# Kernel optimization log

Hardware: AMD Instinct MI355X
Metric: run time of the kernel (lower is better)

The kernel has to match this reference:

```python
import jax, jax.numpy as jnp
import numpy as np

D_HEAD = 64
SCALE = 1.0 / (D_HEAD ** 0.5)
MASK_VALUE = -1e9


def setup_inputs() -> dict:
    key = jax.random.key(0)
    kq, kk, kv, km = jax.random.split(key, 4)
    B, H, S, D = 2, 12, 2048, D_HEAD
    Q = jax.random.normal(kq, (B, H, S, D), dtype=jnp.float32)
    K = jax.random.normal(kk, (B, H, S, D), dtype=jnp.float32)
    V = jax.random.normal(kv, (B, H, S, D), dtype=jnp.float32)
    attn_mask = jax.random.randint(km, (B, 1, S, S), 0, 2).astype(bool)
    return {"Q": Q, "K": K, "V": V, "attn_mask": attn_mask}


def reference(Q, K, V, attn_mask):
    # scores: [B,H,S,S]
    scores = jnp.einsum('bhqd,bhkd->bhqk', Q, K) * SCALE
    scores = jnp.where(attn_mask, MASK_VALUE, scores)
    attn_prob = jax.nn.softmax(scores, axis=-1)
    # dropout p=0.0 (eval mode) -> identity
    context = jnp.einsum('bhqk,bhkd->bhqd', attn_prob, V)
    return (context, attn_prob)
```

## Files before the change

kernel.cpp:

```cpp
#include <hip/hip_runtime.h>
#include <hip/hip_bf16.h>
#include <math.h>

#define B_SZ   2
#define NH     12
#define S_LEN  2048
#define D_HD   64
#define NQ_EL  ((size_t)B_SZ * NH * S_LEN * D_HD)

typedef __attribute__((ext_vector_type(8))) __bf16 bf16x8;
typedef __attribute__((ext_vector_type(4))) __bf16 bf16x4;
typedef __attribute__((ext_vector_type(4))) float  f32x4;
typedef __attribute__((ext_vector_type(4))) unsigned u32x4;

__device__ __forceinline__ int detect_mask_mode64(const void* mask) {
  const int lane = threadIdx.x & 63;
  unsigned v = ((const unsigned*)mask)[lane];
  if (__ballot(v <= 1u) == ~0ull) return 0;
  if (__ballot(v == 0u || v == 0x3f800000u) == ~0ull) return 2;
  unsigned h0 = v & 0xFFFFu, h1 = v >> 16;
  bool okb = (h0 == 0u || h0 == 0x3f80u) && (h1 == 0u || h1 == 0x3f80u);
  if (__ballot(okb) == ~0ull) return 3;
  return 1;
}

__device__ __forceinline__ bool mask_at(const void* mask, int mode, size_t idx) {
  if (mode == 0) return ((const int*)mask)[idx] != 0;
  if (mode == 1) return ((const unsigned char*)mask)[idx] != 0;
  if (mode == 2) return ((const float*)mask)[idx] != 0.0f;
  return ((const unsigned short*)mask)[idx] != 0;
}

__global__ __launch_bounds__(256)
void prep_kernel(const float* __restrict__ Q, const float* __restrict__ K,
                 const float* __restrict__ V, const void* __restrict__ mask,
                 unsigned* __restrict__ bits, __bf16* __restrict__ Qb,
                 __bf16* __restrict__ Kb, __bf16* __restrict__ VT) {
  const int blk = blockIdx.x;
  const int tid = threadIdx.x;
  if (blk < 512) {
    const int mode = detect_mask_mode64(mask);
    const int lane = tid & 63;
#pragma unroll 4
    for (int i = 0; i < 64; ++i) {
      const size_t idx = ((size_t)blk * 64 + i) * 256 + tid;
      const unsigned long long bal = __ballot(mask_at(mask, mode, idx));
      if (lane == 0)       bits[idx >> 5] = (unsigned)bal;
      else if (lane == 32) bits[idx >> 5] = (unsigned)(bal >> 32);
    }
  } else if (blk < 1536) {
    const bool isq = blk < 1024;
    const float* src = isq ? Q : K;
    __bf16* dst = isq ? Qb : Kb;
    const float scale = isq ? 0.125f : 1.0f;
    const size_t base = (size_t)(blk & 511) * 256 + tid;
#pragma unroll
    for (int i = 0; i < 6; ++i) {
      const size_t li = base + (size_t)i * 512 * 256;
      float4 a = ((const float4*)src)[li];
      __bf16 o0 = (__bf16)(a.x * scale), o1 = (__bf16)(a.y * scale);
      __bf16 o2 = (__bf16)(a.z * scale), o3 = (__bf16)(a.w * scale);
      ((ushort4*)dst)[li] = (ushort4){
          __builtin_bit_cast(unsigned short, o0), __builtin_bit_cast(unsigned short, o1),
          __builtin_bit_cast(unsigned short, o2), __builtin_bit_cast(unsigned short, o3)};
    }
  } else {
    __shared__ __align__(16) __bf16 tl[D_HD][72];
    const int t  = blk - 1536;
    const int bh = t >> 5;
    const int k0 = (t & 31) * 64;
#pragma unroll
    for (int i = 0; i < 4; ++i) {
      const int vi = i * 256 + tid;
      const int kk = vi >> 4, dv = (vi & 15) * 4;
      float4 f = *(const float4*)(V + ((size_t)bh * S_LEN + k0 + kk) * D_HD + dv);
      tl[dv + 0][kk] = (__bf16)f.x; tl[dv + 1][kk] = (__bf16)f.y;
      tl[dv + 2][kk] = (__bf16)f.z; tl[dv + 3][kk] = (__bf16)f.w;
    }
    __syncthreads();
#pragma unroll
    for (int half = 0; half < 2; ++half) {
      const int d = half * 32 + (tid >> 3);
      const int kc = (tid & 7) * 8;
      bf16x8 vv = *(const bf16x8*)&tl[d][kc];
      *(bf16x8*)(VT + ((size_t)bh * D_HD + d) * S_LEN + k0 + kc) = vv;
    }
  }
}

__device__ __forceinline__ bf16x8 ld8f(const float* p, float scale) {
  const float4 a = *(const float4*)p;
  const float4 b = *(const float4*)(p + 4);
  bf16x8 r;
  r[0] = (__bf16)(a.x * scale); r[1] = (__bf16)(a.y * scale);
  r[2] = (__bf16)(a.z * scale); r[3] = (__bf16)(a.w * scale);
  r[4] = (__bf16)(b.x * scale); r[5] = (__bf16)(b.y * scale);
  r[6] = (__bf16)(b.z * scale); r[7] = (__bf16)(b.w * scale);
  return r;
}

__global__ __launch_bounds__(512, 4)
void attn_main(const __bf16* __restrict__ Qb, const __bf16* __restrict__ Kb,
               const __bf16* __restrict__ VT, const unsigned* __restrict__ mbits,
               float* __restrict__ out_ctx)
{
  float* out_p = out_ctx + NQ_EL;

  const int flat = blockIdx.x + blockIdx.y * gridDim.x;
  const int wf   = (flat & 7) * 384 + (flat >> 3);
  const int bh   = wf >> 7;
  const int qg   = wf & 127;
  const int b    = bh / NH;

  const int tid  = threadIdx.x;
  const int lane = tid & 63;
  const int w    = tid >> 6;
  const int qbase = qg * 16;
  const int col  = lane & 15;
  const int g    = lane >> 4;
  const int q    = qbase + col;
  const int k0   = w * 256;

  const size_t mbase = ((size_t)b * S_LEN + q) * (S_LEN / 32);

  const size_t qoff = ((size_t)bh * S_LEN + q) * D_HD + g * 8;
  const bf16x8 bq0 = *(const bf16x8*)(Qb + qoff);
  const bf16x8 bq1 = *(const bf16x8*)(Qb + qoff + 32);

  __shared__ float lsh[8][16];
  __shared__ float linv_s[16];
  __shared__ float csum[8][16][66];

  unsigned pe[8][4];
  float lsum = 0.f;
#pragma unroll
  for (int c = 0; c < 8; ++c) {
    const int kc = k0 + c * 32;
    const unsigned mw = mbits[mbase + (kc >> 5)];
    float e[8];
#pragma unroll
    for (int sub = 0; sub < 2; ++sub) {
      const int kb = kc + sub * 16;
      const size_t koff = ((size_t)bh * S_LEN + kb + col) * D_HD + g * 8;
      bf16x8 ak0 = *(const bf16x8*)(Kb + koff);
      bf16x8 ak1 = *(const bf16x8*)(Kb + koff + 32);
      f32x4 acc = {0.f, 0.f, 0.f, 0.f};
      acc = __builtin_amdgcn_mfma_f32_16x16x32_bf16(ak0, bq0, acc, 0, 0, 0);
      acc = __builtin_amdgcn_mfma_f32_16x16x32_bf16(ak1, bq1, acc, 0, 0, 0);
#pragma unroll
      for (int r = 0; r < 4; ++r) {
        const bool msk = (mw >> (sub * 16 + g * 4 + r)) & 1;
        float ev = msk ? 0.f : __expf(acc[r]);
        e[sub * 4 + r] = ev;
        lsum += ev;
      }
    }
#pragma unroll
    for (int j = 0; j < 4; ++j) {
      unsigned lo = __builtin_bit_cast(unsigned short, (__bf16)e[2 * j]);
      unsigned hi = __builtin_bit_cast(unsigned short, (__bf16)e[2 * j + 1]);
      pe[c][j] = (hi << 16) | lo;
    }
  }
  lsum += __shfl_xor(lsum, 16);
  lsum += __shfl_xor(lsum, 32);
  if (lane < 16) lsh[w][col] = lsum;
  __syncthreads();
  float tot = 0.f;
#pragma unroll
  for (int w8 = 0; w8 < 8; ++w8) tot += lsh[w8][col];
  const float inv_l = 1.0f / tot;
  if (w == 0 && lane < 16) linv_s[col] = inv_l;

  f32x4 cacc[4];
#pragma unroll
  for (int dt = 0; dt < 4; dt++) cacc[dt] = (f32x4){0.f, 0.f, 0.f, 0.f};

  float* prow = out_p + (size_t)bh * S_LEN * S_LEN + (size_t)q * S_LEN + k0;
  const __bf16* vbase = VT + (size_t)bh * D_HD * S_LEN;

#pragma unroll
  for (int c = 0; c < 8; ++c) {
    const int kc = k0 + c * 32;
    bf16x8 vf[4];
#pragma unroll
    for (int dt = 0; dt < 4; dt++) {
      const __bf16* vrow = vbase + (size_t)(dt * 16 + col) * S_LEN + kc;
      bf16x4 lo = *(const bf16x4*)(vrow + g * 4);
      bf16x4 hi = *(const bf16x4*)(vrow + 16 + g * 4);
      vf[dt] = __builtin_shufflevector(lo, hi, 0, 1, 2, 3, 4, 5, 6, 7);
    }
#pragma unroll
    for (int sub = 0; sub < 2; ++sub) {
      f32x4 st;
      unsigned u0 = pe[c][sub * 2 + 0], u1 = pe[c][sub * 2 + 1];
      st[0] = __builtin_bit_cast(float, u0 << 16) * inv_l;
      st[1] = __builtin_bit_cast(float, u0 & 0xFFFF0000u) * inv_l;
      st[2] = __builtin_bit_cast(float, u1 << 16) * inv_l;
      st[3] = __builtin_bit_cast(float, u1 & 0xFFFF0000u) * inv_l;
      __builtin_nontemporal_store(st, (f32x4*)(prow + c * 32 + sub * 16 + g * 4));
    }
    u32x4 w4 = {pe[c][0], pe[c][1], pe[c][2], pe[c][3]};
    bf16x8 pa = __builtin_bit_cast(bf16x8, w4);
#pragma unroll
    for (int dt = 0; dt < 4; dt++)
      cacc[dt] = __builtin_amdgcn_mfma_f32_16x16x32_bf16(pa, vf[dt], cacc[dt], 0, 0, 0);
  }

#pragma unroll
  for (int dt = 0; dt < 4; dt++)
#pragma unroll
    for (int r = 0; r < 4; r++)
      csum[w][g * 4 + r][dt * 16 + col] = cacc[dt][r];
  __syncthreads();
  {
    const int qo = tid >> 5;
    const int d0 = (tid * 2) & 63;
    float s0 = 0.f, s1 = 0.f;
#pragma unroll
    for (int w8 = 0; w8 < 8; ++w8) {
      s0 += csum[w8][qo][d0];
      s1 += csum[w8][qo][d0 + 1];
    }
    const float lv = linv_s[qo];
    float2 o = {s0 * lv, s1 * lv};
    *(float2*)(out_ctx + ((size_t)bh * S_LEN + qbase + qo) * D_HD + d0) = o;
  }
}

template<bool USE_BITS>
__global__ __launch_bounds__(512)
void attn_fb(const float* __restrict__ Qg, const float* __restrict__ Kg,
             const float* __restrict__ Vg, const void* __restrict__ mask,
             const unsigned* __restrict__ mbits, float* __restrict__ out_ctx)
{
  float* out_p = out_ctx + NQ_EL;
  const int flat = blockIdx.x + blockIdx.y * gridDim.x;
  const int wf   = (flat & 7) * 96 + (flat >> 3);
  const int qt = wf & 31, bh = wf >> 5, b = bh / NH;
  const int tid = threadIdx.x, lane = tid & 63, w = tid >> 6;
  const int qw = w & 3, kh = w >> 2;
  const int qbase = qt * 64 + qw * 16;
  const int col = lane & 15, g = lane >> 4;
  const int q = qbase + col;
  const int k0 = kh * (S_LEN / 2);
  int mmode = 0;
  if constexpr (!USE_BITS) mmode = detect_mask_mode64(mask);
  const size_t mrow  = (size_t)b * S_LEN * S_LEN;
  const size_t mbase = ((size_t)b * S_LEN + q) * (S_LEN / 32);
  const size_t qoff = ((size_t)bh * S_LEN + q) * D_HD + g * 8;
  const bf16x8 bq0 = ld8f(Qg + qoff, 0.125f);
  const bf16x8 bq1 = ld8f(Qg + qoff + 32, 0.125f);

  float lsum = 0.f;
  for (int kc = k0; kc < k0 + S_LEN / 2; kc += 32) {
    unsigned mw = 0;
    if constexpr (USE_BITS) mw = mbits[mbase + (kc >> 5)];
#pragma unroll
    for (int sub = 0; sub < 2; ++sub) {
      const int kb = kc + sub * 16;
      const size_t koff = ((size_t)bh * S_LEN + kb + col) * D_HD + g * 8;
      bf16x8 ak0 = ld8f(Kg + koff, 1.0f);
      bf16x8 ak1 = ld8f(Kg + koff + 32, 1.0f);
      f32x4 acc = {0.f, 0.f, 0.f, 0.f};
      acc = __builtin_amdgcn_mfma_f32_16x16x32_bf16(ak0, bq0, acc, 0, 0, 0);
      acc = __builtin_amdgcn_mfma_f32_16x16x32_bf16(ak1, bq1, acc, 0, 0, 0);
#pragma unroll
      for (int r = 0; r < 4; ++r) {
        bool msk;
        if constexpr (USE_BITS) msk = (mw >> (sub * 16 + g * 4 + r)) & 1;
        else msk = mask_at(mask, mmode, mrow + (size_t)q * S_LEN + kb + g * 4 + r);
        lsum += msk ? 0.f : __expf(acc[r]);
      }
    }
  }
  lsum += __shfl_xor(lsum, 16);
  lsum += __shfl_xor(lsum, 32);
  __shared__ float lsh[8][16];
  __shared__ float csum[4][16][66];
  if (lane < 16) lsh[w][col] = lsum;
  __syncthreads();
  const float inv_l = 1.0f / (lsum + lsh[w ^ 4][col]);

  f32x4 cacc[4];
#pragma unroll
  for (int dt = 0; dt < 4; dt++) cacc[dt] = (f32x4){0.f, 0.f, 0.f, 0.f};
  float* prow = out_p + (size_t)bh * S_LEN * S_LEN + (size_t)q * S_LEN;

  for (int it = 0; it < S_LEN / 64; ++it) {
    const int kc = k0 + it * 32;
    unsigned mw = 0;
    if constexpr (USE_BITS) mw = mbits[mbase + (kc >> 5)];
    float p[8];
#pragma unroll
    for (int sub = 0; sub < 2; ++sub) {
      const int kb = kc + sub * 16;
      const size_t koff = ((size_t)bh * S_LEN + kb + col) * D_HD + g * 8;
      bf16x8 ak0 = ld8f(Kg + koff, 1.0f);
      bf16x8 ak1 = ld8f(Kg + koff + 32, 1.0f);
      f32x4 acc = {0.f, 0.f, 0.f, 0.f};
      acc = __builtin_amdgcn_mfma_f32_16x16x32_bf16(ak0, bq0, acc, 0, 0, 0);
      acc = __builtin_amdgcn_mfma_f32_16x16x32_bf16(ak1, bq1, acc, 0, 0, 0);
#pragma unroll
      for (int r = 0; r < 4; ++r) {
        bool msk;
        if constexpr (USE_BITS) msk = (mw >> (sub * 16 + g * 4 + r)) & 1;
        else msk = mask_at(mask, mmode, mrow + (size_t)q * S_LEN + kb + g * 4 + r);
        p[sub * 4 + r] = msk ? 0.f : __expf(acc[r]) * inv_l;
      }
      float4 st = {p[sub * 4 + 0], p[sub * 4 + 1], p[sub * 4 + 2], p[sub * 4 + 3]};
      *(float4*)(prow + kb + g * 4) = st;
    }
    bf16x8 pa;
#pragma unroll
    for (int e = 0; e < 8; e++) pa[e] = (__bf16)p[e];
#pragma unroll
    for (int dt = 0; dt < 4; dt++) {
      bf16x8 vf;
#pragma unroll
      for (int e = 0; e < 8; e++) {
        const int kidx = kc + (e >> 2) * 16 + g * 4 + (e & 3);
        vf[e] = (__bf16)Vg[((size_t)bh * S_LEN + kidx) * D_HD + dt * 16 + col];
      }
      cacc[dt] = __builtin_amdgcn_mfma_f32_16x16x32_bf16(pa, vf, cacc[dt], 0, 0, 0);
    }
  }
  if (kh == 1) {
#pragma unroll
    for (int dt = 0; dt < 4; dt++)
#pragma unroll
      for (int r = 0; r < 4; r++)
        csum[qw][g * 4 + r][dt * 16 + col] = cacc[dt][r];
  }
  __syncthreads();
  if (kh == 0) {
#pragma unroll
    for (int dt = 0; dt < 4; dt++)
#pragma unroll
      for (int r = 0; r < 4; r++)
        out_ctx[((size_t)bh * S_LEN + qbase + g * 4 + r) * D_HD + dt * 16 + col] =
            cacc[dt][r] + csum[qw][g * 4 + r][dt * 16 + col];
  }
}

__global__ __launch_bounds__(256)
void build_bits_kernel(const void* __restrict__ mask, unsigned* __restrict__ bits) {
  const int mode = detect_mask_mode64(mask);
  const size_t i = (size_t)blockIdx.x * 256 + threadIdx.x;
  const unsigned long long bal = __ballot(mask_at(mask, mode, i));
  const int lane = threadIdx.x & 63;
  if (lane == 0)       bits[i >> 5] = (unsigned)bal;
  else if (lane == 32) bits[i >> 5] = (unsigned)(bal >> 32);
}

extern "C" void kernel_launch(void* const* d_in, const int* in_sizes, int n_in,
                              void* d_out, int out_size, void* d_ws, size_t ws_size,
                              hipStream_t stream) {
  const float* Q = (const float*)d_in[0];
  const float* K = (const float*)d_in[1];
  const float* V = (const float*)d_in[2];
  const void* mask = d_in[3];
  float* out = (float*)d_out;

  const size_t mask_elems = (size_t)B_SZ * S_LEN * S_LEN;
  const size_t off_bits = 256;
  const size_t off_q  = off_bits + mask_elems / 8;
  const size_t off_k  = off_q + NQ_EL * 2;
  const size_t off_vt = off_k + NQ_EL * 2;
  const size_t need   = off_vt + NQ_EL * 2;

  if (ws_size >= need) {
    unsigned* bits = (unsigned*)((char*)d_ws + off_bits);
    __bf16* Qb = (__bf16*)((char*)d_ws + off_q);
    __bf16* Kb = (__bf16*)((char*)d_ws + off_k);
    __bf16* VT = (__bf16*)((char*)d_ws + off_vt);
    prep_kernel<<<2304, 256, 0, stream>>>(Q, K, V, mask, bits, Qb, Kb, VT);
    dim3 grid(128, 24);
    attn_main<<<grid, 512, 0, stream>>>(Qb, Kb, VT, bits, out);
  } else if (ws_size >= off_q) {
    unsigned* bits = (unsigned*)((char*)d_ws + off_bits);
    build_bits_kernel<<<(unsigned)(mask_elems / 256), 256, 0, stream>>>(mask, bits);
    dim3 gfb(S_LEN / 64, B_SZ * NH);
    attn_fb<true><<<gfb, 512, 0, stream>>>(Q, K, V, mask, bits, out);
  } else {
    dim3 gfb(S_LEN / 64, B_SZ * NH);
    attn_fb<false><<<gfb, 512, 0, stream>>>(Q, K, V, mask, nullptr, out);
  }
}
```

Baseline: 327.5 us.

## Prefetch K tiles one chunk ahead and coalesce attn_prob stores via lane shuffles

K fragments and mask words for the next 32-key chunk are now loaded one iteration early, so global-load latency overlaps the current chunk's MFMAs and exps. The probability write-out is reorganized: lanes exchange packed bf16 values with shuffles so that eight consecutive lanes write 128 contiguous bytes of one query row, replacing strided 16-byte stores that were scattered across 16 rows. The stores also change from nontemporal to regular. This costs extra shuffles, extra registers for the prefetched tiles, and recomputed per-row inverse sums.

```diff
diff --git a/kernel.cpp b/kernel.cpp
--- a/kernel.cpp
+++ b/kernel.cpp
@@ -99,6 +99,13 @@
   return r;
 }
 
+__device__ __forceinline__ float bflo(unsigned u) {
+  return __builtin_bit_cast(float, u << 16);
+}
+__device__ __forceinline__ float bfhi(unsigned u) {
+  return __builtin_bit_cast(float, u & 0xFFFF0000u);
+}
+
 __global__ __launch_bounds__(512, 4)
 void attn_main(const __bf16* __restrict__ Qb, const __bf16* __restrict__ Kb,
                const __bf16* __restrict__ VT, const unsigned* __restrict__ mbits,
@@ -122,8 +129,9 @@
   const int k0   = w * 256;
 
   const size_t mbase = ((size_t)b * S_LEN + q) * (S_LEN / 32);
-
-  const size_t qoff = ((size_t)bh * S_LEN + q) * D_HD + g * 8;
+  const size_t khead = (size_t)bh * S_LEN;
+
+  const size_t qoff = (khead + q) * D_HD + g * 8;
   const bf16x8 bq0 = *(const bf16x8*)(Qb + qoff);
   const bf16x8 bq1 = *(const bf16x8*)(Qb + qoff + 32);
 
@@ -133,26 +141,53 @@
 
   unsigned pe[8][4];
   float lsum = 0.f;
+
+  bf16x8 nk0a, nk0b, nk1a, nk1b;
+  {
+    const size_t koff0 = (khead + k0 + col) * D_HD + g * 8;
+    const size_t koff1 = (khead + k0 + 16 + col) * D_HD + g * 8;
+    nk0a = *(const bf16x8*)(Kb + koff0);
+    nk0b = *(const bf16x8*)(Kb + koff0 + 32);
+    nk1a = *(const bf16x8*)(Kb + koff1);
+    nk1b = *(const bf16x8*)(Kb + koff1 + 32);
+  }
+  unsigned nmw = mbits[mbase + (k0 >> 5)];
+
 #pragma unroll
   for (int c = 0; c < 8; ++c) {
-    const int kc = k0 + c * 32;
-    const unsigned mw = mbits[mbase + (kc >> 5)];
+    const bf16x8 k0a = nk0a, k0b = nk0b, k1a = nk1a, k1b = nk1b;
+    const unsigned mw = nmw;
+    if (c < 7) {
+      const int kn = k0 + (c + 1) * 32;
+      const size_t koff0 = (khead + kn + col) * D_HD + g * 8;
+      const size_t koff1 = (khead + kn + 16 + col) * D_HD + g * 8;
+      nk0a = *(const bf16x8*)(Kb + koff0);
+      nk0b = *(const bf16x8*)(Kb + koff0 + 32);
+      nk1a = *(const bf16x8*)(Kb + koff1);
+      nk1b = *(const bf16x8*)(Kb + koff1 + 32);
+      nmw = mbits[mbase + (kn >> 5)];
+    }
     float e[8];
-#pragma unroll
-    for (int sub = 0; sub < 2; ++sub) {
-      const int kb = kc + sub * 16;
-      const size_t koff = ((size_t)bh * S_LEN + kb + col) * D_HD + g * 8;
-      bf16x8 ak0 = *(const bf16x8*)(Kb + koff);
-      bf16x8 ak1 = *(const bf16x8*)(Kb + koff + 32);
+    {
       f32x4 acc = {0.f, 0.f, 0.f, 0.f};
-      acc = __builtin_amdgcn_mfma_f32_16x16x32_bf16(ak0, bq0, acc, 0, 0, 0);
-      acc = __builtin_amdgcn_mfma_f32_16x16x32_bf16(ak1, bq1, acc, 0, 0, 0);
+      acc = __builtin_amdgcn_mfma_f32_16x16x32_bf16(k0a, bq0, acc, 0, 0, 0);
+      acc = __builtin_amdgcn_mfma_f32_16x16x32_bf16(k0b, bq1, acc, 0, 0, 0);
 #pragma unroll
       for (int r = 0; r < 4; ++r) {
-        const bool msk = (mw >> (sub * 16 + g * 4 + r)) & 1;
-        float ev = msk ? 0.f : __expf(acc[r]);
-        e[sub * 4 + r] = ev;
-        lsum += ev;
+        const bool msk = (mw >> (g * 4 + r)) & 1;
+        e[r] = msk ? 0.f : __expf(acc[r]);
+        lsum += e[r];
+      }
+    }
+    {
+      f32x4 acc = {0.f, 0.f, 0.f, 0.f};
+      acc = __builtin_amdgcn_mfma_f32_16x16x32_bf16(k1a, bq0, acc, 0, 0, 0);
+      acc = __builtin_amdgcn_mfma_f32_16x16x32_bf16(k1b, bq1, acc, 0, 0, 0);
+#pragma unroll
+      for (int r = 0; r < 4; ++r) {
+        const bool msk = (mw >> (16 + g * 4 + r)) & 1;
+        e[4 + r] = msk ? 0.f : __expf(acc[r]);
+        lsum += e[4 + r];
       }
     }
 #pragma unroll
@@ -166,17 +201,29 @@
   lsum += __shfl_xor(lsum, 32);
   if (lane < 16) lsh[w][col] = lsum;
   __syncthreads();
-  float tot = 0.f;
-#pragma unroll
-  for (int w8 = 0; w8 < 8; ++w8) tot += lsh[w8][col];
-  const float inv_l = 1.0f / tot;
-  if (w == 0 && lane < 16) linv_s[col] = inv_l;
+  {
+    float tot = 0.f;
+#pragma unroll
+    for (int w8 = 0; w8 < 8; ++w8) tot += lsh[w8][col];
+    if (w == 0 && lane < 16) linv_s[col] = 1.0f / tot;
+  }
+  const int Lr = lane >> 3;
+  const int u  = lane & 7;
+  float linv_t[2];
+#pragma unroll
+  for (int t = 0; t < 2; ++t) {
+    float tot = 0.f;
+#pragma unroll
+    for (int w8 = 0; w8 < 8; ++w8) tot += lsh[w8][t * 8 + Lr];
+    linv_t[t] = 1.0f / tot;
+  }
+  const int subg = u >> 2;
 
   f32x4 cacc[4];
 #pragma unroll
   for (int dt = 0; dt < 4; dt++) cacc[dt] = (f32x4){0.f, 0.f, 0.f, 0.f};
 
-  float* prow = out_p + (size_t)bh * S_LEN * S_LEN + (size_t)q * S_LEN + k0;
+  float* pblk = out_p + (size_t)bh * S_LEN * S_LEN + (size_t)qbase * S_LEN + k0;
   const __bf16* vbase = VT + (size_t)bh * D_HD * S_LEN;
 
 #pragma unroll
@@ -191,14 +238,17 @@
       vf[dt] = __builtin_shufflevector(lo, hi, 0, 1, 2, 3, 4, 5, 6, 7);
     }
 #pragma unroll
-    for (int sub = 0; sub < 2; ++sub) {
-      f32x4 st;
-      unsigned u0 = pe[c][sub * 2 + 0], u1 = pe[c][sub * 2 + 1];
-      st[0] = __builtin_bit_cast(float, u0 << 16) * inv_l;
-      st[1] = __builtin_bit_cast(float, u0 & 0xFFFF0000u) * inv_l;
-      st[2] = __builtin_bit_cast(float, u1 << 16) * inv_l;
-      st[3] = __builtin_bit_cast(float, u1 & 0xFFFF0000u) * inv_l;
-      __builtin_nontemporal_store(st, (f32x4*)(prow + c * 32 + sub * 16 + g * 4));
+    for (int t = 0; t < 2; ++t) {
+      const int src = 16 * (u & 3) + t * 8 + Lr;
+      unsigned a0 = (unsigned)__shfl((int)pe[c][0], src);
+      unsigned a1 = (unsigned)__shfl((int)pe[c][1], src);
+      unsigned a2 = (unsigned)__shfl((int)pe[c][2], src);
+      unsigned a3 = (unsigned)__shfl((int)pe[c][3], src);
+      const unsigned lo = subg ? a2 : a0;
+      const unsigned hi = subg ? a3 : a1;
+      const float lv = linv_t[t];
+      f32x4 st = {bflo(lo) * lv, bfhi(lo) * lv, bflo(hi) * lv, bfhi(hi) * lv};
+      *(f32x4*)(pblk + (size_t)(t * 8 + Lr) * S_LEN + c * 32 + u * 4) = st;
     }
     u32x4 w4 = {pe[c][0], pe[c][1], pe[c][2], pe[c][3]};
     bf16x8 pa = __builtin_bit_cast(bf16x8, w4);
```

Measured after the change: 334.0 us. +2.0%, slower.

## Stage unnormalized probabilities in LDS to write full contiguous rows per wave

Applied to the files above, without the earlier changes.

Unnormalized bf16 exponentials are now staged in a shared-memory buffer, aliased with the csum reduction buffer. Each wave then writes two full probability rows of 2048 floats with fully contiguous 16-byte stores, replacing the scattered per-lane 16-byte nontemporal stores spread across 16 rows. The goal is better write coalescing for the dominant S×S probability output. The cost is about 66KB of LDS per block, which may cut occupancy below the launch-bounds target, plus an extra barrier. The nontemporal hint is also dropped.

```diff
diff --git a/kernel.cpp b/kernel.cpp
--- a/kernel.cpp
+++ b/kernel.cpp
@@ -7,6 +7,7 @@
 #define S_LEN  2048
 #define D_HD   64
 #define NQ_EL  ((size_t)B_SZ * NH * S_LEN * D_HD)
+#define EST    2056
 
 typedef __attribute__((ext_vector_type(8))) __bf16 bf16x8;
 typedef __attribute__((ext_vector_type(4))) __bf16 bf16x4;
@@ -99,6 +100,13 @@
   return r;
 }
 
+__device__ __forceinline__ float bflo(unsigned u) {
+  return __builtin_bit_cast(float, u << 16);
+}
+__device__ __forceinline__ float bfhi(unsigned u) {
+  return __builtin_bit_cast(float, u & 0xFFFF0000u);
+}
+
 __global__ __launch_bounds__(512, 4)
 void attn_main(const __bf16* __restrict__ Qb, const __bf16* __restrict__ Kb,
                const __bf16* __restrict__ VT, const unsigned* __restrict__ mbits,
@@ -122,14 +130,17 @@
   const int k0   = w * 256;
 
   const size_t mbase = ((size_t)b * S_LEN + q) * (S_LEN / 32);
-
-  const size_t qoff = ((size_t)bh * S_LEN + q) * D_HD + g * 8;
+  const size_t khead = (size_t)bh * S_LEN;
+
+  const size_t qoff = (khead + q) * D_HD + g * 8;
   const bf16x8 bq0 = *(const bf16x8*)(Qb + qoff);
   const bf16x8 bq1 = *(const bf16x8*)(Qb + qoff + 32);
 
+  __shared__ __align__(16) unsigned char shraw[16 * EST * 2];
+  auto ebuf = (unsigned short (*)[EST])shraw;
+  auto csum = (float (*)[16][66])shraw;
   __shared__ float lsh[8][16];
   __shared__ float linv_s[16];
-  __shared__ float csum[8][16][66];
 
   unsigned pe[8][4];
   float lsum = 0.f;
@@ -141,7 +152,7 @@
 #pragma unroll
     for (int sub = 0; sub < 2; ++sub) {
       const int kb = kc + sub * 16;
-      const size_t koff = ((size_t)bh * S_LEN + kb + col) * D_HD + g * 8;
+      const size_t koff = (khead + kb + col) * D_HD + g * 8;
       bf16x8 ak0 = *(const bf16x8*)(Kb + koff);
       bf16x8 ak1 = *(const bf16x8*)(Kb + koff + 32);
       f32x4 acc = {0.f, 0.f, 0.f, 0.f};
@@ -161,52 +172,65 @@
       unsigned hi = __builtin_bit_cast(unsigned short, (__bf16)e[2 * j + 1]);
       pe[c][j] = (hi << 16) | lo;
     }
+    unsigned long long v01 = (unsigned long long)pe[c][0] |
+                             ((unsigned long long)pe[c][1] << 32);
+    unsigned long long v23 = (unsigned long long)pe[c][2] |
+                             ((unsigned long long)pe[c][3] << 32);
+    *(unsigned long long*)&ebuf[col][kc + g * 4]      = v01;
+    *(unsigned long long*)&ebuf[col][kc + 16 + g * 4] = v23;
   }
   lsum += __shfl_xor(lsum, 16);
   lsum += __shfl_xor(lsum, 32);
   if (lane < 16) lsh[w][col] = lsum;
   __syncthreads();
-  float tot = 0.f;
-#pragma unroll
-  for (int w8 = 0; w8 < 8; ++w8) tot += lsh[w8][col];
-  const float inv_l = 1.0f / tot;
-  if (w == 0 && lane < 16) linv_s[col] = inv_l;
+
+  {
+    float tot = 0.f;
+#pragma unroll
+    for (int w8 = 0; w8 < 8; ++w8) tot += lsh[w8][col];
+    if (w == 0 && lane < 16) linv_s[col] = 1.0f / tot;
+  }
+
+#pragma unroll
+  for (int j = 0; j < 2; ++j) {
+    const int rr = w * 2 + j;
+    float tot = 0.f;
+#pragma unroll
+    for (int w8 = 0; w8 < 8; ++w8) tot += lsh[w8][rr];
+    const float lv = 1.0f / tot;
+    float* prow = out_p + (size_t)bh * S_LEN * S_LEN +
+                  (size_t)(qbase + rr) * S_LEN;
+#pragma unroll
+    for (int i = 0; i < 8; ++i) {
+      const int k = i * 256 + lane * 4;
+      unsigned long long v = *(const unsigned long long*)&ebuf[rr][k];
+      const unsigned u0 = (unsigned)v, u1 = (unsigned)(v >> 32);
+      f32x4 st = {bflo(u0) * lv, bfhi(u0) * lv, bflo(u1) * lv, bfhi(u1) * lv};
+      *(f32x4*)(prow + k) = st;
+    }
+  }
 
   f32x4 cacc[4];
 #pragma unroll
   for (int dt = 0; dt < 4; dt++) cacc[dt] = (f32x4){0.f, 0.f, 0.f, 0.f};
-
-  float* prow = out_p + (size_t)bh * S_LEN * S_LEN + (size_t)q * S_LEN + k0;
   const __bf16* vbase = VT + (size_t)bh * D_HD * S_LEN;
 
 #pragma unroll
   for (int c = 0; c < 8; ++c) {
     const int kc = k0 + c * 32;
-    bf16x8 vf[4];
+    u32x4 w4 = {pe[c][0], pe[c][1], pe[c][2], pe[c][3]};
+    bf16x8 pa = __builtin_bit_cast(bf16x8, w4);
 #pragma unroll
     for (int dt = 0; dt < 4; dt++) {
       const __bf16* vrow = vbase + (size_t)(dt * 16 + col) * S_LEN + kc;
       bf16x4 lo = *(const bf16x4*)(vrow + g * 4);
       bf16x4 hi = *(const bf16x4*)(vrow + 16 + g * 4);
-      vf[dt] = __builtin_shufflevector(lo, hi, 0, 1, 2, 3, 4, 5, 6, 7);
-    }
-#pragma unroll
-    for (int sub = 0; sub < 2; ++sub) {
-      f32x4 st;
-      unsigned u0 = pe[c][sub * 2 + 0], u1 = pe[c][sub * 2 + 1];
-      st[0] = __builtin_bit_cast(float, u0 << 16) * inv_l;
-      st[1] = __builtin_bit_cast(float, u0 & 0xFFFF0000u) * inv_l;
-      st[2] = __builtin_bit_cast(float, u1 << 16) * inv_l;
-      st[3] = __builtin_bit_cast(float, u1 & 0xFFFF0000u) * inv_l;
-      __builtin_nontemporal_store(st, (f32x4*)(prow + c * 32 + sub * 16 + g * 4));
-    }
-    u32x4 w4 = {pe[c][0], pe[c][1], pe[c][2], pe[c][3]};
-    bf16x8 pa = __builtin_bit_cast(bf16x8, w4);
-#pragma unroll
-    for (int dt = 0; dt < 4; dt++)
-      cacc[dt] = __builtin_amdgcn_mfma_f32_16x16x32_bf16(pa, vf[dt], cacc[dt], 0, 0, 0);
-  }
-
+      bf16x8 vf = __builtin_shufflevector(lo, hi, 0, 1, 2, 3, 4, 5, 6, 7);
+      cacc[dt] = __builtin_amdgcn_mfma_f32_16x16x32_bf16(pa, vf, cacc[dt], 0, 0, 0);
+    }
+  }
+
+  __syncthreads();
 #pragma unroll
   for (int dt = 0; dt < 4; dt++)
 #pragma unroll
```

Measured after the change: 347.6 us. +6.1%, slower.
